# Optimization experiments

Measured on AMD Instinct MI355X. Metric: run time of the kernel, lower is better.

## Reference

```python
import math
import jax, jax.numpy as jnp
import numpy as np

B, T, C, H = 2, 2048, 1024, 16
MAX_SEQ = 2048


def _make_pe(max_seq: int, dim: int, base: float = 10000.0) -> np.ndarray:
    pe = np.zeros((max_seq, dim), dtype=np.float32)
    position = np.arange(max_seq, dtype=np.float32)[:, None]
    div_term = np.exp(np.arange(0, dim, 2, dtype=np.float32) * (-math.log(base) / dim))
    pe[:, 0::2] = np.sin(position * div_term)
    pe[:, 1::2] = np.cos(position * div_term)
    return pe


def setup_inputs() -> dict:
    key = jax.random.key(0)
    k1, k2, k3 = jax.random.split(key, 3)
    x = jax.random.normal(k1, (B, T, C), dtype=jnp.float32)
    # torch Linear default init scale ~ 1/sqrt(fan_in)
    w_qkv = jax.random.normal(k2, (3 * C, C), dtype=jnp.float32) / math.sqrt(C)
    w_proj = jax.random.normal(k3, (C, C), dtype=jnp.float32) / math.sqrt(C)
    pe = jnp.asarray(_make_pe(MAX_SEQ, C))
    return {"x": x, "w_qkv": w_qkv, "w_proj": w_proj, "pe": pe}


def reference(x, w_qkv, w_proj, pe):
    b, t, c = x.shape
    h = H
    d = c // h
    # RoPE module adds sinusoidal PE under torch.no_grad() -> stop_gradient
    xp = jax.lax.stop_gradient(x + pe[None, :t, :])
    qkv = xp @ w_qkv.T  # [b, t, 3c]
    q, k, v = jnp.split(qkv, 3, axis=-1)
    q = q.reshape(b, t, h, d).transpose(0, 2, 1, 3)  # bhtd
    k = k.reshape(b, t, h, d).transpose(0, 2, 1, 3)
    v = v.reshape(b, t, h, d).transpose(0, 2, 1, 3)
    att = jnp.einsum("bhqd,bhkd->bhqk", q, k) * (1.0 / math.sqrt(d))
    causal = jnp.tril(jnp.ones((t, t), dtype=bool))  # [t, t]
    att = jnp.where(causal[None, None], att, -jnp.inf)
    att = jax.nn.softmax(att, axis=-1)
    y = jnp.einsum("bhqk,bhkd->bhqd", att, v)
    y = y.transpose(0, 2, 1, 3).reshape(b, t, c)
    return y @ w_proj.T
```

## Files before the change

kernel.cpp:

```cpp
#include <hip/hip_runtime.h>
#include <cstdint>

typedef __bf16 bf16x8 __attribute__((ext_vector_type(8)));
typedef __bf16 bf16x4 __attribute__((ext_vector_type(4)));
typedef float  f32x4  __attribute__((ext_vector_type(4)));

static constexpr int kB = 2, kT = 2048, kC = 1024, kH = 16, kD = 64;
static constexpr int kK = 1024;

__device__ __forceinline__ uint16_t f2bf(float f) {
  uint32_t u = __builtin_bit_cast(uint32_t, f);
  u += 0x7FFFu + ((u >> 16) & 1u);
  return (uint16_t)(u >> 16);
}

__device__ __forceinline__ void gl_lds16(const void* g, void* l) {
  __builtin_amdgcn_global_load_lds((__attribute__((address_space(1))) void*)(void*)g,
                                   (__attribute__((address_space(3))) void*)l, 16, 0, 0);
}

__global__ __launch_bounds__(256) void prep_all(const float* __restrict__ x,
                                                const float* __restrict__ pe,
                                                const float* __restrict__ wqkv,
                                                const float* __restrict__ wproj,
                                                uint16_t* __restrict__ xp,
                                                uint16_t* __restrict__ wq,
                                                uint16_t* __restrict__ wp) {
  constexpr int NX = kB * kT * kC / 4;
  constexpr int NWQ = 3 * kC * kC / 4;
  const int i = blockIdx.x * 256 + threadIdx.x;
  if (i < NX) {
    const float4 xv = ((const float4*)x)[i];
    const int c4 = i & (kC / 4 - 1);
    const int t = (i / (kC / 4)) & (kT - 1);
    const float4 pv = ((const float4*)pe)[t * (kC / 4) + c4];
    ushort4 o;
    o.x = f2bf(xv.x + pv.x);
    o.y = f2bf(xv.y + pv.y);
    o.z = f2bf(xv.z + pv.z);
    o.w = f2bf(xv.w + pv.w);
    ((ushort4*)xp)[i] = o;
  } else if (i < NX + NWQ) {
    const int j = i - NX;
    const float4 v = ((const float4*)wqkv)[j];
    ushort4 u;
    u.x = f2bf(v.x); u.y = f2bf(v.y); u.z = f2bf(v.z); u.w = f2bf(v.w);
    ((ushort4*)wq)[j] = u;
  } else {
    const int j = i - NX - NWQ;
    const float4 v = ((const float4*)wproj)[j];
    ushort4 u;
    u.x = f2bf(v.x); u.y = f2bf(v.y); u.z = f2bf(v.z); u.w = f2bf(v.w);
    ((ushort4*)wp)[j] = u;
  }
}

__global__ __launch_bounds__(512, 2) void gemm_qkv(const uint16_t* __restrict__ A,
                                                   const uint16_t* __restrict__ W,
                                                   uint16_t* __restrict__ qb,
                                                   uint16_t* __restrict__ kb,
                                                   uint16_t* __restrict__ vT) {
  __shared__ __align__(1024) char lds[131072];
  const int tid = threadIdx.x;
  const int lane = tid & 63;
  const int wid = tid >> 6;
  const int l15 = lane & 15, l4 = lane >> 4;
  const int WM = wid >> 2, WN = wid & 3;
  const int orig = (int)blockIdx.x;
  const int xcd = orig & 7, j = orig >> 3;
  const int m0 = (xcd * 2 + (j & 1)) * 256;
  const int n0 = (j >> 1) * 256;

  f32x4 acc[2][4][4] = {};
  bf16x8 bfp[2][4];

  auto stage = [&](int isA, int buf, int kt) {
#pragma unroll
    for (int c = 0; c < 4; ++c) {
      const int off = (c * 512 + tid) * 16;
      const int lr = off >> 7, cbl = off & 127;
      const size_t grow = (size_t)((isA ? m0 : n0) + lr) * kK + kt * 64;
      gl_lds16((const char*)(isA ? A : W) + grow * 2 + (cbl ^ ((lr & 7) << 4)),
               lds + (isA ? 0 : 65536) + buf * 32768 + off);
    }
  };

#define QKV_PHASE(CBUF, H, SA, SBUF, KT, VM)                                      \
  {                                                                               \
    stage(SA, SBUF, KT);                                                          \
    if (VM == 4)                                                                  \
      asm volatile("s_waitcnt vmcnt(4)" ::: "memory");                            \
    else                                                                          \
      asm volatile("s_waitcnt vmcnt(8)" ::: "memory");                            \
    __builtin_amdgcn_s_barrier();                                                 \
    asm volatile("" ::: "memory");                                                \
    const char* Ab = lds + (CBUF)*32768;                                          \
    const char* Bb = lds + 65536 + (CBUF)*32768;                                  \
    if ((H) == 0) {                                                               \
      _Pragma("unroll") for (int ks = 0; ks < 2; ++ks)                            \
          _Pragma("unroll") for (int nt = 0; nt < 4; ++nt) {                      \
        const int lr = WN * 64 + nt * 16 + l15;                                   \
        bfp[ks][nt] = *(const bf16x8*)(Bb + lr * 128 +                            \
                                       ((ks * 64 + l4 * 16) ^ ((lr & 7) << 4)));  \
      }                                                                           \
    }                                                                             \
    _Pragma("unroll") for (int ks = 0; ks < 2; ++ks) {                            \
      bf16x8 af[4];                                                               \
      _Pragma("unroll") for (int mt = 0; mt < 4; ++mt) {                          \
        const int lr = (H)*128 + WM * 64 + mt * 16 + l15;                         \
        af[mt] = *(const bf16x8*)(Ab + lr * 128 +                                 \
                                  ((ks * 64 + l4 * 16) ^ ((lr & 7) << 4)));       \
      }                                                                           \
      __builtin_amdgcn_s_setprio(1);                                              \
      _Pragma("unroll") for (int mt = 0; mt < 4; ++mt)                            \
          _Pragma("unroll") for (int nt = 0; nt < 4; ++nt)                        \
              acc[H][mt][nt] = __builtin_amdgcn_mfma_f32_16x16x32_bf16(           \
                  af[mt], bfp[ks][nt], acc[H][mt][nt], 0, 0, 0);                  \
      __builtin_amdgcn_s_setprio(0);                                              \
    }                                                                             \
    asm volatile("" ::: "memory");                                                \
    __builtin_amdgcn_s_barrier();                                                 \
    asm volatile("" ::: "memory");                                                \
  }

  stage(1, 0, 0);
  stage(0, 0, 0);

  for (int i = 0; i < 8; ++i) {
    const int ktb1 = 2 * i + 1;
    const int ktb0 = (2 * i + 2 > 15) ? 15 : 2 * i + 2;
    QKV_PHASE(0, 0, 1, 1, ktb1, 4);
    QKV_PHASE(0, 1, 0, 1, ktb1, 8);
    QKV_PHASE(1, 0, 1, 0, ktb0, 4);
    QKV_PHASE(1, 1, 0, 0, ktb0, 8);
  }
  asm volatile("s_waitcnt vmcnt(0)" ::: "memory");
  __builtin_amdgcn_s_barrier();
  asm volatile("" ::: "memory");

  const int sec = n0 >> 10;
  const int b = m0 >> 11, tb = m0 & (kT - 1);
  if (sec < 2) {
    uint16_t* dst = (sec == 0) ? qb : kb;
#pragma unroll
    for (int h = 0; h < 2; ++h)
#pragma unroll
      for (int mt = 0; mt < 4; ++mt)
#pragma unroll
        for (int nt = 0; nt < 4; ++nt)
#pragma unroll
          for (int r = 0; r < 4; ++r) {
            const int m = h * 128 + WM * 64 + mt * 16 + l4 * 4 + r;
            const int nn = (n0 & (kC - 1)) + WN * 64 + nt * 16 + l15;
            const int hh = nn >> 6, d = nn & 63;
            dst[((size_t)((b * kH + hh) * kT + tb + m)) * kD + d] =
                f2bf(acc[h][mt][nt][r]);
          }
  } else {
#pragma unroll
    for (int h = 0; h < 2; ++h)
#pragma unroll
      for (int mt = 0; mt < 4; ++mt)
#pragma unroll
        for (int nt = 0; nt < 4; ++nt) {
          const int nl = WN * 64 + nt * 16 + l15;
          const int mb2 = (h * 128 + WM * 64 + mt * 16 + l4 * 4) * 2;
          ushort4 pk;
          pk.x = f2bf(acc[h][mt][nt][0]);
          pk.y = f2bf(acc[h][mt][nt][1]);
          pk.z = f2bf(acc[h][mt][nt][2]);
          pk.w = f2bf(acc[h][mt][nt][3]);
          *(ushort4*)(lds + nl * 512 + (mb2 ^ ((nl & 7) << 4))) = pk;
        }
    asm volatile("" ::: "memory");
    __builtin_amdgcn_s_barrier();
    asm volatile("" ::: "memory");
#pragma unroll
    for (int it = 0; it < 16; ++it) {
      const int chunk = it * 512 + tid;
      const int nr = chunk >> 5, mb = (chunk & 31) * 16;
      const bf16x8 v = *(const bf16x8*)(lds + nr * 512 + (mb ^ ((nr & 7) << 4)));
      const int nn = (n0 - 2048) + nr;
      const int hh = nn >> 6, d = nn & 63;
      *(bf16x8*)(vT + ((size_t)((b * kH + hh) * kD + d)) * kT + tb + (chunk & 31) * 8) = v;
    }
  }
#undef QKV_PHASE
}

__global__ __launch_bounds__(256, 2) void gemm_proj(const uint16_t* __restrict__ A,
                                                    const uint16_t* __restrict__ W,
                                                    float* __restrict__ out) {
  __shared__ __align__(1024) char lds[65536];
  const int tid = threadIdx.x;
  const int lane = tid & 63;
  const int wid = tid >> 6;
  const int l15 = lane & 15, l4 = lane >> 4;
  const int WM = wid >> 1, WN = wid & 1;
  const int orig = (int)blockIdx.x;
  const int xcd = orig & 7, j = orig >> 3;
  const int m0 = (xcd * 4 + (j & 3)) * 128;
  const int n0 = (j >> 2) * 128;

  f32x4 acc[2][2][4] = {};
  bf16x8 bfp[2][4];

  auto stage = [&](int isA, int buf, int kt) {
#pragma unroll
    for (int c = 0; c < 4; ++c) {
      const int off = (c * 256 + tid) * 16;
      const int lr = off >> 7, cbl = off & 127;
      const size_t grow = (size_t)((isA ? m0 : n0) + lr) * kK + kt * 64;
      gl_lds16((const char*)(isA ? A : W) + grow * 2 + (cbl ^ ((lr & 7) << 4)),
               lds + (isA ? 0 : 32768) + buf * 16384 + off);
    }
  };

#define PRJ_PHASE(CBUF, H, SA, SBUF, KT, VM)                                      \
  {                                                                               \
    stage(SA, SBUF, KT);                                                          \
    if (VM == 4)                                                                  \
      asm volatile("s_waitcnt vmcnt(4)" ::: "memory");                            \
    else                                                                          \
      asm volatile("s_waitcnt vmcnt(8)" ::: "memory");                            \
    __builtin_amdgcn_s_barrier();                                                 \
    asm volatile("" ::: "memory");                                                \
    const char* Ab = lds + (CBUF)*16384;                                          \
    const char* Bb = lds + 32768 + (CBUF)*16384;                                  \
    if ((H) == 0) {                                                               \
      _Pragma("unroll") for (int ks = 0; ks < 2; ++ks)                            \
          _Pragma("unroll") for (int nt = 0; nt < 4; ++nt) {                      \
        const int lr = WN * 64 + nt * 16 + l15;                                   \
        bfp[ks][nt] = *(const bf16x8*)(Bb + lr * 128 +                            \
                                       ((ks * 64 + l4 * 16) ^ ((lr & 7) << 4)));  \
      }                                                                           \
    }                                                                             \
    _Pragma("unroll") for (int ks = 0; ks < 2; ++ks) {                            \
      bf16x8 af[2];                                                               \
      _Pragma("unroll") for (int mt = 0; mt < 2; ++mt) {                          \
        const int lr = (H)*64 + WM * 32 + mt * 16 + l15;                          \
        af[mt] = *(const bf16x8*)(Ab + lr * 128 +                                 \
                                  ((ks * 64 + l4 * 16) ^ ((lr & 7) << 4)));       \
      }                                                                           \
      __builtin_amdgcn_s_setprio(1);                                              \
      _Pragma("unroll") for (int mt = 0; mt < 2; ++mt)                            \
          _Pragma("unroll") for (int nt = 0; nt < 4; ++nt)                        \
              acc[H][mt][nt] = __builtin_amdgcn_mfma_f32_16x16x32_bf16(           \
                  af[mt], bfp[ks][nt], acc[H][mt][nt], 0, 0, 0);                  \
      __builtin_amdgcn_s_setprio(0);                                              \
    }                                                                             \
    asm volatile("" ::: "memory");                                                \
    __builtin_amdgcn_s_barrier();                                                 \
    asm volatile("" ::: "memory");                                                \
  }

  stage(1, 0, 0);
  stage(0, 0, 0);

  for (int i = 0; i < 8; ++i) {
    const int ktb1 = 2 * i + 1;
    const int ktb0 = (2 * i + 2 > 15) ? 15 : 2 * i + 2;
    PRJ_PHASE(0, 0, 1, 1, ktb1, 4);
    PRJ_PHASE(0, 1, 0, 1, ktb1, 8);
    PRJ_PHASE(1, 0, 1, 0, ktb0, 4);
    PRJ_PHASE(1, 1, 0, 0, ktb0, 8);
  }
  asm volatile("s_waitcnt vmcnt(0)" ::: "memory");
  __builtin_amdgcn_s_barrier();
  asm volatile("" ::: "memory");

#pragma unroll
  for (int h = 0; h < 2; ++h)
#pragma unroll
    for (int mt = 0; mt < 2; ++mt)
#pragma unroll
      for (int nt = 0; nt < 4; ++nt)
#pragma unroll
        for (int r = 0; r < 4; ++r) {
          const int m = m0 + h * 64 + WM * 32 + mt * 16 + l4 * 4 + r;
          const int n = n0 + WN * 64 + nt * 16 + l15;
          out[(size_t)m * kC + n] = acc[h][mt][nt][r];
        }
#undef PRJ_PHASE
}

__global__ __launch_bounds__(256, 4) void attn(const uint16_t* __restrict__ qb,
                                               const uint16_t* __restrict__ kb,
                                               const uint16_t* __restrict__ vT,
                                               uint16_t* __restrict__ y) {
  __shared__ __align__(1024) char lds[40960];
  const int lane = threadIdx.x & 63;
  const int wid = threadIdx.x >> 6;
  const int l15 = lane & 15, l4 = lane >> 4;
  const int bh = blockIdx.x;
  const int qt = (int)(gridDim.y - 1) - (int)blockIdx.y;
  const int q0 = qt * 64 + wid * 16;
  const size_t base = (size_t)bh * kT * kD;
  const uint16_t* Q = qb + base;
  const uint16_t* Kp = kb + base;
  const uint16_t* Vt = vT + base;
  char* P = lds + 32768 + wid * 2048;
  const int xr = (l15 & 7) << 4;

  bf16x8 qf[2];
#pragma unroll
  for (int ks = 0; ks < 2; ++ks) {
    bf16x8 t = *(const bf16x8*)(Q + (size_t)(q0 + l15) * kD + ks * 32 + l4 * 8);
#pragma unroll
    for (int i = 0; i < 8; ++i) t[i] = (__bf16)((float)t[i] * 0.1803368801f);
    qf[ks] = t;
  }
  bf16x8 ones;
#pragma unroll
  for (int i = 0; i < 8; ++i) ones[i] = (__bf16)1.0f;

  float m_ = -1e30f;
  f32x4 o[4];
  f32x4 ol = {0.f, 0.f, 0.f, 0.f};
#pragma unroll
  for (int nt = 0; nt < 4; ++nt) o[nt] = (f32x4){0.f, 0.f, 0.f, 0.f};

  const int nkt = qt + 1;

  auto STAGE = [&](int bi, int k0) {
#pragma unroll
    for (int c = 0; c < 2; ++c) {
      const int call = wid * 2 + c;
      const int row = call * 8 + (lane >> 3);
      const int colb = (((lane & 7) ^ ((lane >> 3) & 7)) << 4);
      gl_lds16((const char*)Kp + ((size_t)(k0 + row) * kD) * 2 + colb,
               lds + bi * 8192 + call * 1024);
      gl_lds16((const char*)Vt + ((size_t)row * kT + k0) * 2 + colb,
               lds + 16384 + bi * 8192 + call * 1024);
    }
  };

  int cur = 0;
  STAGE(0, 0);
  for (int kt = 0; kt < nkt; ++kt) {
    const int k0 = kt * 64;
    asm volatile("s_waitcnt vmcnt(0)" ::: "memory");
    __builtin_amdgcn_s_barrier();
    asm volatile("" ::: "memory");
    if (kt + 1 < nkt) STAGE(cur ^ 1, k0 + 64);

    const char* Kb = lds + cur * 8192;
    const char* Vb = lds + 16384 + cur * 8192;

    f32x4 s[4] = {};
    __builtin_amdgcn_s_setprio(1);
#pragma unroll
    for (int ks = 0; ks < 2; ++ks)
#pragma unroll
      for (int nt = 0; nt < 4; ++nt) {
        const bf16x8 kf =
            *(const bf16x8*)(Kb + (nt * 16 + l15) * 128 + ((ks * 64 + l4 * 16) ^ xr));
        s[nt] = __builtin_amdgcn_mfma_f32_16x16x32_bf16(kf, qf[ks], s[nt], 0, 0, 0);
      }
    __builtin_amdgcn_s_setprio(0);

    if (kt == nkt - 1) {
      const int qq = q0 + l15;
#pragma unroll
      for (int nt = 0; nt < 4; ++nt)
#pragma unroll
        for (int r = 0; r < 4; ++r)
          if (k0 + nt * 16 + l4 * 4 + r > qq) s[nt][r] = -1e30f;
    }

    float pm = s[0][0];
#pragma unroll
    for (int nt = 0; nt < 4; ++nt)
#pragma unroll
      for (int r = 0; r < 4; ++r) pm = fmaxf(pm, s[nt][r]);
    if (!__all(pm <= m_ + 11.0f)) {
      float rm = fmaxf(pm, __shfl_xor(pm, 16));
      rm = fmaxf(rm, __shfl_xor(rm, 32));
      const float newm = fmaxf(m_, rm);
      const float sc = exp2f(m_ - newm);
      m_ = newm;
#pragma unroll
      for (int nt = 0; nt < 4; ++nt)
#pragma unroll
        for (int r = 0; r < 4; ++r) o[nt][r] *= sc;
#pragma unroll
      for (int r = 0; r < 4; ++r) ol[r] *= sc;
    }
#pragma unroll
    for (int nt = 0; nt < 4; ++nt)
#pragma unroll
      for (int r = 0; r < 4; ++r) s[nt][r] = exp2f(s[nt][r] - m_);

#pragma unroll
    for (int nt = 0; nt < 4; ++nt) {
      bf16x4 pk;
#pragma unroll
      for (int r = 0; r < 4; ++r) pk[r] = (__bf16)s[nt][r];
      *(bf16x4*)(P + l15 * 128 + ((nt * 32 + l4 * 8) ^ xr)) = pk;
    }
    asm volatile("s_waitcnt lgkmcnt(0)" ::: "memory");
    __builtin_amdgcn_sched_barrier(0);

    bf16x8 pf[2];
#pragma unroll
    for (int ks = 0; ks < 2; ++ks)
      pf[ks] = *(const bf16x8*)(P + l15 * 128 + ((ks * 64 + l4 * 16) ^ xr));
    __builtin_amdgcn_s_setprio(1);
#pragma unroll
    for (int ks = 0; ks < 2; ++ks) {
#pragma unroll
      for (int nt = 0; nt < 4; ++nt) {
        const bf16x8 vf =
            *(const bf16x8*)(Vb + (nt * 16 + l15) * 128 + ((ks * 64 + l4 * 16) ^ xr));
        o[nt] = __builtin_amdgcn_mfma_f32_16x16x32_bf16(vf, pf[ks], o[nt], 0, 0, 0);
      }
      ol = __builtin_amdgcn_mfma_f32_16x16x32_bf16(ones, pf[ks], ol, 0, 0, 0);
    }
    __builtin_amdgcn_s_setprio(0);

    cur ^= 1;
  }

  const float inv = 1.0f / ol[0];
  const int b = bh >> 4, h = bh & 15;
  const int q = q0 + l15;
#pragma unroll
  for (int nt = 0; nt < 4; ++nt) {
    bf16x4 yv;
#pragma unroll
    for (int r = 0; r < 4; ++r) yv[r] = (__bf16)(o[nt][r] * inv);
    *(bf16x4*)(y + ((size_t)(b * kT + q)) * kC + h * kD + nt * 16 + l4 * 4) = yv;
  }
}

extern "C" void kernel_launch(void* const* d_in, const int* in_sizes, int n_in,
                              void* d_out, int out_size, void* d_ws, size_t ws_size,
                              hipStream_t stream) {
  const float* x = (const float*)d_in[0];
  const float* wqkv = (const float*)d_in[1];
  const float* wproj = (const float*)d_in[2];
  const float* pe = (const float*)d_in[3];

  char* ws = (char*)d_ws;
  uint16_t* xp = (uint16_t*)(ws);
  uint16_t* wq = (uint16_t*)(ws + (size_t)(8u << 20));
  uint16_t* wp = (uint16_t*)(ws + (size_t)(14u << 20));
  uint16_t* qbuf = (uint16_t*)(ws + (size_t)(16u << 20));
  uint16_t* kbuf = (uint16_t*)(ws + (size_t)(24u << 20));
  uint16_t* vTb = (uint16_t*)(ws + (size_t)(32u << 20));

  prep_all<<<dim3(8192), 256, 0, stream>>>(x, pe, wqkv, wproj, xp, wq, wp);

  gemm_qkv<<<dim3(192), 512, 0, stream>>>(xp, wq, qbuf, kbuf, vTb);

  attn<<<dim3(kB * kH, kT / 64), 256, 0, stream>>>(qbuf, kbuf, vTb, xp);

  gemm_proj<<<dim3(256), 256, 0, stream>>>(xp, wp, (float*)d_out);
}
```

Baseline: 100.8 us.

## Replace half-tile phased QKV GEMM pipeline with simple per-k double buffering

The QKV GEMM main loop drops the four-phase macro schedule, which split each K-tile into two M-halves with separate barriers and staggered A/B staging. It now uses one iteration per K-tile: it prefetches both A and B for the next tile into the other buffer, waits, and computes a 128x64 warp tile (8x4 MFMAs) against freshly loaded B fragments. The warp-to-M mapping also changes so each warp owns 128 contiguous rows. This halves the number of barriers and simplifies scheduling. The cost is coarser overlap between loads and MFMA work and register pressure from re-loading B fragments every tile.

Result: slower. 104.2 us (+3.3%).

```diff
diff --git a/kernel.cpp b/kernel.cpp
--- a/kernel.cpp
+++ b/kernel.cpp
@@ -71,8 +71,7 @@
   const int m0 = (xcd * 2 + (j & 1)) * 256;
   const int n0 = (j >> 1) * 256;
 
-  f32x4 acc[2][4][4] = {};
-  bf16x8 bfp[2][4];
+  f32x4 acc[8][4] = {};
 
   auto stage = [&](int isA, int buf, int kt) {
 #pragma unroll
@@ -85,54 +84,44 @@
     }
   };
 
-#define QKV_PHASE(CBUF, H, SA, SBUF, KT, VM)                                      \
-  {                                                                               \
-    stage(SA, SBUF, KT);                                                          \
-    if (VM == 4)                                                                  \
-      asm volatile("s_waitcnt vmcnt(4)" ::: "memory");                            \
-    else                                                                          \
-      asm volatile("s_waitcnt vmcnt(8)" ::: "memory");                            \
-    __builtin_amdgcn_s_barrier();                                                 \
-    asm volatile("" ::: "memory");                                                \
-    const char* Ab = lds + (CBUF)*32768;                                          \
-    const char* Bb = lds + 65536 + (CBUF)*32768;                                  \
-    if ((H) == 0) {                                                               \
-      _Pragma("unroll") for (int ks = 0; ks < 2; ++ks)                            \
-          _Pragma("unroll") for (int nt = 0; nt < 4; ++nt) {                      \
-        const int lr = WN * 64 + nt * 16 + l15;                                   \
-        bfp[ks][nt] = *(const bf16x8*)(Bb + lr * 128 +                            \
-                                       ((ks * 64 + l4 * 16) ^ ((lr & 7) << 4)));  \
-      }                                                                           \
-    }                                                                             \
-    _Pragma("unroll") for (int ks = 0; ks < 2; ++ks) {                            \
-      bf16x8 af[4];                                                               \
-      _Pragma("unroll") for (int mt = 0; mt < 4; ++mt) {                          \
-        const int lr = (H)*128 + WM * 64 + mt * 16 + l15;                         \
-        af[mt] = *(const bf16x8*)(Ab + lr * 128 +                                 \
-                                  ((ks * 64 + l4 * 16) ^ ((lr & 7) << 4)));       \
-      }                                                                           \
-      __builtin_amdgcn_s_setprio(1);                                              \
-      _Pragma("unroll") for (int mt = 0; mt < 4; ++mt)                            \
-          _Pragma("unroll") for (int nt = 0; nt < 4; ++nt)                        \
-              acc[H][mt][nt] = __builtin_amdgcn_mfma_f32_16x16x32_bf16(           \
-                  af[mt], bfp[ks][nt], acc[H][mt][nt], 0, 0, 0);                  \
-      __builtin_amdgcn_s_setprio(0);                                              \
-    }                                                                             \
-    asm volatile("" ::: "memory");                                                \
-    __builtin_amdgcn_s_barrier();                                                 \
-    asm volatile("" ::: "memory");                                                \
-  }
-
   stage(1, 0, 0);
   stage(0, 0, 0);
 
-  for (int i = 0; i < 8; ++i) {
-    const int ktb1 = 2 * i + 1;
-    const int ktb0 = (2 * i + 2 > 15) ? 15 : 2 * i + 2;
-    QKV_PHASE(0, 0, 1, 1, ktb1, 4);
-    QKV_PHASE(0, 1, 0, 1, ktb1, 8);
-    QKV_PHASE(1, 0, 1, 0, ktb0, 4);
-    QKV_PHASE(1, 1, 0, 0, ktb0, 8);
+  for (int kt = 0; kt < 16; ++kt) {
+    const int cur = kt & 1;
+    const int ktn = (kt + 1 > 15) ? 15 : kt + 1;
+    stage(1, cur ^ 1, ktn);
+    stage(0, cur ^ 1, ktn);
+    asm volatile("s_waitcnt vmcnt(8)" ::: "memory");
+    __builtin_amdgcn_s_barrier();
+    asm volatile("" ::: "memory");
+    const char* Ab = lds + cur * 32768;
+    const char* Bb = lds + 65536 + cur * 32768;
+#pragma unroll
+    for (int ks = 0; ks < 2; ++ks) {
+      bf16x8 bf[4];
+#pragma unroll
+      for (int nt = 0; nt < 4; ++nt) {
+        const int lr = WN * 64 + nt * 16 + l15;
+        bf[nt] = *(const bf16x8*)(Bb + lr * 128 +
+                                  ((ks * 64 + l4 * 16) ^ ((lr & 7) << 4)));
+      }
+#pragma unroll
+      for (int mt = 0; mt < 8; ++mt) {
+        const int lr = WM * 128 + mt * 16 + l15;
+        const bf16x8 af = *(const bf16x8*)(Ab + lr * 128 +
+                                           ((ks * 64 + l4 * 16) ^ ((lr & 7) << 4)));
+        __builtin_amdgcn_s_setprio(1);
+#pragma unroll
+        for (int nt = 0; nt < 4; ++nt)
+          acc[mt][nt] = __builtin_amdgcn_mfma_f32_16x16x32_bf16(af, bf[nt],
+                                                                acc[mt][nt], 0, 0, 0);
+        __builtin_amdgcn_s_setprio(0);
+      }
+    }
+    asm volatile("" ::: "memory");
+    __builtin_amdgcn_s_barrier();
+    asm volatile("" ::: "memory");
   }
   asm volatile("s_waitcnt vmcnt(0)" ::: "memory");
   __builtin_amdgcn_s_barrier();
@@ -143,35 +132,31 @@
   if (sec < 2) {
     uint16_t* dst = (sec == 0) ? qb : kb;
 #pragma unroll
-    for (int h = 0; h < 2; ++h)
-#pragma unroll
-      for (int mt = 0; mt < 4; ++mt)
-#pragma unroll
-        for (int nt = 0; nt < 4; ++nt)
-#pragma unroll
-          for (int r = 0; r < 4; ++r) {
-            const int m = h * 128 + WM * 64 + mt * 16 + l4 * 4 + r;
-            const int nn = (n0 & (kC - 1)) + WN * 64 + nt * 16 + l15;
-            const int hh = nn >> 6, d = nn & 63;
-            dst[((size_t)((b * kH + hh) * kT + tb + m)) * kD + d] =
-                f2bf(acc[h][mt][nt][r]);
-          }
+    for (int mt = 0; mt < 8; ++mt)
+#pragma unroll
+      for (int nt = 0; nt < 4; ++nt)
+#pragma unroll
+        for (int r = 0; r < 4; ++r) {
+          const int m = WM * 128 + mt * 16 + l4 * 4 + r;
+          const int nn = (n0 & (kC - 1)) + WN * 64 + nt * 16 + l15;
+          const int hh = nn >> 6, d = nn & 63;
+          dst[((size_t)((b * kH + hh) * kT + tb + m)) * kD + d] =
+              f2bf(acc[mt][nt][r]);
+        }
   } else {
 #pragma unroll
-    for (int h = 0; h < 2; ++h)
-#pragma unroll
-      for (int mt = 0; mt < 4; ++mt)
-#pragma unroll
-        for (int nt = 0; nt < 4; ++nt) {
-          const int nl = WN * 64 + nt * 16 + l15;
-          const int mb2 = (h * 128 + WM * 64 + mt * 16 + l4 * 4) * 2;
-          ushort4 pk;
-          pk.x = f2bf(acc[h][mt][nt][0]);
-          pk.y = f2bf(acc[h][mt][nt][1]);
-          pk.z = f2bf(acc[h][mt][nt][2]);
-          pk.w = f2bf(acc[h][mt][nt][3]);
-          *(ushort4*)(lds + nl * 512 + (mb2 ^ ((nl & 7) << 4))) = pk;
-        }
+    for (int mt = 0; mt < 8; ++mt)
+#pragma unroll
+      for (int nt = 0; nt < 4; ++nt) {
+        const int nl = WN * 64 + nt * 16 + l15;
+        const int mb2 = (WM * 128 + mt * 16 + l4 * 4) * 2;
+        ushort4 pk;
+        pk.x = f2bf(acc[mt][nt][0]);
+        pk.y = f2bf(acc[mt][nt][1]);
+        pk.z = f2bf(acc[mt][nt][2]);
+        pk.w = f2bf(acc[mt][nt][3]);
+        *(ushort4*)(lds + nl * 512 + (mb2 ^ ((nl & 7) << 4))) = pk;
+      }
     asm volatile("" ::: "memory");
     __builtin_amdgcn_s_barrier();
     asm volatile("" ::: "memory");
@@ -185,7 +170,6 @@
       *(bf16x8*)(vT + ((size_t)((b * kH + hh) * kD + d)) * kT + tb + (chunk & 31) * 8) = v;
     }
   }
-#undef QKV_PHASE
 }
 
 __global__ __launch_bounds__(256, 2) void gemm_proj(const uint16_t* __restrict__ A,
```
